# Performance work log

Hardware: AMD Instinct MI355X
Metric: run time of the kernel (lower is better)

## Reference

```python
import jax, jax.numpy as jnp
import numpy as np
from jax import lax

B, C, H, W = 256, 64, 48, 48   # batch, in_channels, spatial_dim, spatial_dim
E = 5                           # num_experts (ConditionalConv2D default)
DIM = 64 + 1                    # n_regulators + 1


def setup_inputs() -> dict:
    key = jax.random.key(0)
    ks = jax.random.split(key, 24)
    def n(k, shape, s=0.05):
        return jax.random.normal(k, shape, jnp.float32) * s
    inp = {
        "spatial_maps": jax.random.normal(ks[0], (B, C, H, W), jnp.float32),
        "cluster_info": jax.random.randint(ks[1], (B,), 0, C),
        # ConditionalConv2D (1x1, num_experts=5)
        "expert_w": n(ks[2], (E, C, C)),          # [experts, out_c, in_c] (1x1 squeezed)
        "cond_b": n(ks[3], (C,)),
        "route_emb": n(ks[4], (C, 4 * C)),        # Embedding(num_clusters=C, pool_emb=4C)
        "route_W": n(ks[5], (E, 8 * C)),          # Linear(2*pool_emb -> E)
        "route_b": n(ks[6], (E,)),
        # weight-normed conv stack (v, g, bias, prelu-a)
        "v1": n(ks[7], (32, C, 3, 3)),  "g1": jnp.ones((32,), jnp.float32),  "cb1": n(ks[8], (32,)),  "a1": jnp.array(0.1, jnp.float32),
        "v2": n(ks[9], (64, 32, 3, 3)), "g2": jnp.ones((64,), jnp.float32),  "cb2": n(ks[10], (64,)), "a2": jnp.array(0.1, jnp.float32),
        "v3": n(ks[11], (128, 64, 3, 3)), "g3": jnp.ones((128,), jnp.float32), "cb3": n(ks[12], (128,)), "a3": jnp.array(0.1, jnp.float32),
        # cluster embedding + alpha + MLP
        "emb2": n(ks[13], (C, 128)),
        "alpha": jnp.array(1.0, jnp.float32),
        "mW1": n(ks[14], (64, 128)), "mb1": n(ks[15], (64,)), "a4": jnp.array(0.1, jnp.float32),
        "mW2": n(ks[16], (32, 64)),  "mb2": n(ks[17], (32,)), "a5": jnp.array(0.1, jnp.float32),
        "mW3": n(ks[18], (DIM, 32)), "mb3": n(ks[19], (DIM,)),
    }
    return inp


def _wn(v, g):
    # weight_norm over all dims except 0 (torch default dim=0)
    nrm = jnp.sqrt((v * v).sum((1, 2, 3)))
    return v * (g / nrm)[:, None, None, None]


def _conv(x, w, b):
    y = lax.conv_general_dilated(x, w, (1, 1), 'SAME',
                                 dimension_numbers=('NCHW', 'OIHW', 'NCHW'))
    return y + b[None, :, None, None]


def _prelu(x, a):
    return jnp.where(x >= 0, x, a * x)


def _mpool(x):
    return lax.reduce_window(x, -jnp.inf, lax.max, (1, 1, 2, 2), (1, 1, 2, 2), 'VALID')


def reference(spatial_maps, cluster_info, expert_w, cond_b, route_emb, route_W, route_b,
              v1, g1, cb1, a1, v2, g2, cb2, a2, v3, g3, cb3, a3,
              emb2, alpha, mW1, mb1, a4, mW2, mb2, a5, mW3, mb3):
    x = spatial_maps
    # routing: adaptive avg pool (2,2), flatten, concat cluster embedding, linear, sigmoid
    pooled = x.reshape(B, C, 2, H // 2, 2, W // 2).mean((3, 5)).reshape(B, 4 * C)
    feat = jnp.concatenate([pooled, route_emb[cluster_info]], axis=1)      # [B, 8C]
    rw = jax.nn.sigmoid(feat @ route_W.T + route_b)                        # [B, E]
    # per-sample expert-mixed 1x1 kernel, applied as batched 1x1 conv
    kern = jnp.einsum('be,eoi->boi', rw, expert_w)                         # [B, C, C]
    cc = jnp.einsum('boi,bihw->bohw', kern, x) + cond_b[None, :, None, None]
    out = jax.nn.sigmoid(cc) * x                                           # attention gate
    # dense conv stack
    h = _mpool(_prelu(_conv(out, _wn(v1, g1), cb1), a1))
    h = _mpool(_prelu(_conv(h, _wn(v2, g2), cb2), a2))
    h = _mpool(_prelu(_conv(h, _wn(v3, g3), cb3), a3))
    h = h.mean((2, 3))                                                      # AdaptiveAvgPool2d(1)+Flatten -> [B,128]
    h = h + emb2[cluster_info] * alpha
    # MLP head
    h = _prelu(h @ mW1.T + mb1, a4)
    h = _prelu(h @ mW2.T + mb2, a5)
    return h @ mW3.T + mb3                                                  # [B, DIM]
```

## Files before the change

### kernel.cpp

```cpp
#include <hip/hip_runtime.h>


typedef _Float16 f16;
typedef f16 f16x8 __attribute__((ext_vector_type(8)));
typedef f16 f16x4 __attribute__((ext_vector_type(4)));
typedef f16 f16x2 __attribute__((ext_vector_type(2)));
typedef __fp16 h16x2 __attribute__((ext_vector_type(2)));
typedef float f32x4 __attribute__((ext_vector_type(4)));

constexpr size_t OFF_POOLED = 0;
constexpr size_t OFF_KERN   = 65536;
constexpr size_t OFF_W1     = 65536 + 1048576;
constexpr size_t OFF_W2     = OFF_W1 + 32*64*12;
constexpr size_t OFF_W3     = OFF_W2 + 64*32*12;
constexpr size_t OFF_H1     = OFF_W3 + 128*64*12;

__device__ __forceinline__ float sigmoidf_(float z) {
    return __builtin_amdgcn_rcpf(1.0f + __expf(-z));
}

__device__ __forceinline__ f16x2 pkrtz(float a, float b) {
    h16x2 r = __builtin_amdgcn_cvt_pkrtz(a, b);
    f16x2 o; o[0] = (f16)r[0]; o[1] = (f16)r[1];
    return o;
}

__device__ __forceinline__ void store_slot8(f16* glds, int row, int sc, int icg, const float* c) {
    f16x2 p0 = pkrtz(c[0], c[1]);
    f16x2 p1 = pkrtz(c[2], c[3]);
    f16x2 p2 = pkrtz(c[4], c[5]);
    f16x2 p3 = pkrtz(c[6], c[7]);
    f16x8 hv = { p0[0], p0[1], p1[0], p1[1], p2[0], p2[1], p3[0], p3[1] };
    *(f16x8*)&glds[(row * 50 + sc) * 64 + ((icg ^ (sc & 7)) << 3)] = hv;
}

__global__ void __launch_bounds__(256)
k_prep(const float* __restrict__ x,
       const float* __restrict__ v1, const float* __restrict__ g1,
       const float* __restrict__ v2, const float* __restrict__ g2,
       const float* __restrict__ v3, const float* __restrict__ g3,
       float* __restrict__ ws)
{
    const int blk = blockIdx.x;
    const int lane = threadIdx.x & 63;
    const int w = threadIdx.x >> 6;
    if (blk < 4096) {
        const int slab = blk * 4 + w;
        const float4* p = (const float4*)(x + (size_t)slab * 2304);
        float a0 = 0.f, a1 = 0.f, a2 = 0.f, a3 = 0.f;
        #pragma unroll
        for (int j = 0; j < 9; j++) {
            int i = lane + 64 * j;
            int row = i / 12, cg = i - 12 * row;
            float4 v = p[i];
            float s = v.x + v.y + v.z + v.w;
            bool hq = (row >= 24), wq = (cg >= 6);
            a0 += (!hq && !wq) ? s : 0.f;
            a1 += (!hq &&  wq) ? s : 0.f;
            a2 += ( hq && !wq) ? s : 0.f;
            a3 += ( hq &&  wq) ? s : 0.f;
        }
        #pragma unroll
        for (int off = 32; off; off >>= 1) {
            a0 += __shfl_down(a0, off);
            a1 += __shfl_down(a1, off);
            a2 += __shfl_down(a2, off);
            a3 += __shfl_down(a3, off);
        }
        if (lane == 0) {
            int b = slab >> 6, c = slab & 63;
            float* d = ws + OFF_POOLED + (size_t)b * 256 + c * 4;
            d[0] = a0 * (1.0f / 576.0f);
            d[1] = a1 * (1.0f / 576.0f);
            d[2] = a2 * (1.0f / 576.0f);
            d[3] = a3 * (1.0f / 576.0f);
        }
    } else {
        int bo = (blk - 4096) * 4 + w;
        const float* v; const float* g; int IC, oc; int which;
        if (bo < 32)       { v = v1; g = g1; oc = bo;      IC = 64; which = 1; }
        else if (bo < 96)  { v = v2; g = g2; oc = bo - 32; IC = 32; which = 2; }
        else               { v = v3; g = g3; oc = bo - 96; IC = 64; which = 3; }
        int n = IC * 9;
        const float* vo = v + (size_t)oc * n;
        float s = 0.0f;
        for (int i = lane; i < n; i += 64) { float xv = vo[i]; s += xv * xv; }
        #pragma unroll
        for (int off = 32; off; off >>= 1) s += __shfl_down(s, off);
        float tot = __shfl(s, 0);
        float sc = g[oc] / sqrtf(tot);
        if (which == 1) {
            f16* o1 = (f16*)(ws + OFF_W1);
            for (int i = lane; i < n; i += 64) {
                int ic = i / 9, kk = i - ic * 9;
                o1[kk * 2048 + oc * 64 + (ic ^ ((oc & 7) << 3))] = (f16)(vo[i] * sc);
            }
        } else if (which == 2) {
            f16* o2 = (f16*)(ws + OFF_W2);
            for (int i = lane; i < n; i += 64) {
                int ic = i / 9, kk = i - ic * 9;
                o2[(kk * 64 + oc) * 32 + ic] = (f16)(vo[i] * sc);
            }
        } else {
            f16* o3 = (f16*)(ws + OFF_W3);
            for (int i = lane; i < n; i += 64) {
                int ic = i / 9, kk = i - ic * 9;
                o3[(kk * 128 + oc) * 64 + ic] = (f16)(vo[i] * sc);
            }
        }
    }
}

__global__ void k_route(const int* __restrict__ cluster,
                        const float* __restrict__ route_emb,
                        const float* __restrict__ route_W,
                        const float* __restrict__ route_b,
                        const float* __restrict__ expert_w,
                        float* __restrict__ ws)
{
    int b = blockIdx.x, t = threadIdx.x;
    __shared__ float feat[512];
    __shared__ float rwv[5];
    __shared__ float red[256];
    int cl = cluster[b];
    feat[t]       = ws[OFF_POOLED + (size_t)b * 256 + t];
    feat[256 + t] = route_emb[(size_t)cl * 256 + t];
    __syncthreads();
    float f0 = feat[t], f1 = feat[256 + t];
    for (int e = 0; e < 5; e++) {
        float pv = f0 * route_W[e * 512 + t] + f1 * route_W[e * 512 + 256 + t];
        red[t] = pv;
        __syncthreads();
        if (t < 128) red[t] += red[t + 128];
        __syncthreads();
        if (t < 64) {
            float s = red[t] + red[t + 64];
            #pragma unroll
            for (int off = 32; off; off >>= 1) s += __shfl_down(s, off);
            if (t == 0) rwv[e] = 1.0f / (1.0f + __expf(-(s + route_b[e])));
        }
        __syncthreads();
    }
    float r0 = rwv[0], r1 = rwv[1], r2 = rwv[2], r3 = rwv[3], r4 = rwv[4];
    f16* khg = (f16*)(ws + OFF_KERN);
    for (int j = t; j < 4096; j += 256) {
        int oc = j >> 6, ic = j & 63;
        float kv = r0 * expert_w[j] + r1 * expert_w[4096 + j] +
                   r2 * expert_w[2 * 4096 + j] + r3 * expert_w[3 * 4096 + j] +
                   r4 * expert_w[4 * 4096 + j];
        khg[(size_t)b * 4096 + oc * 64 + (ic ^ ((oc & 7) << 3))] = (f16)kv;
    }
}

__global__ void __launch_bounds__(512, 4)
k_f1(const float* __restrict__ x, const f16* __restrict__ kernH,
     const float* __restrict__ cond_b, const f16* __restrict__ w1H,
     const float* __restrict__ cb1, const float* __restrict__ a1,
     f16* __restrict__ h1h)
{
    extern __shared__ char smem[];
    f16*  glds  = (f16*)smem;
    f16*  kh    = (f16*)(smem + 64000);
    float* cbl  = (float*)(smem + 72192);
    f16*  hm    = (f16*)smem;

    const int t = threadIdx.x;
    const int tile = blockIdx.x;
    const int b = blockIdx.y;
    const int r0 = tile * 8;
    const int w = t >> 6, l = t & 63;
    const int l15 = l & 15, agrp = l >> 4;

    ((uint4*)kh)[t] = ((const uint4*)(kernH + (size_t)b * 4096))[t];
    if (t < 64) cbl[t] = cond_b[t];
    if (t < 160) {
        int row = t >> 4, rem = t & 15;
        int col = (rem >= 8) ? 49 : 0;
        int slot = rem & 7;
        uint4 z = {};
        *(uint4*)&glds[(row * 50 + col) * 64 + slot * 8] = z;
    }
    for (int e = t; e < 960; e += 512) {
        int row = e / 96;
        int rem = e - row * 96;
        int colg = rem >> 3;
        int icg = rem & 7;
        int r_in = r0 - 1 + row;
        float4 va[8];
        if (r_in >= 0 && r_in < 48) {
            const float4* xp = (const float4*)x + ((size_t)(b * 64 + icg * 8)) * 576 + r_in * 12 + colg;
            #pragma unroll
            for (int i = 0; i < 8; i++) va[i] = xp[i * 576];
        } else {
            #pragma unroll
            for (int i = 0; i < 8; i++) va[i] = (float4){0.f, 0.f, 0.f, 0.f};
        }
        float c0[8], c1[8], c2c[8], c3[8];
        #pragma unroll
        for (int i = 0; i < 8; i++) { c0[i] = va[i].x; c1[i] = va[i].y; c2c[i] = va[i].z; c3[i] = va[i].w; }
        int scb = colg * 4 + 1;
        store_slot8(glds, row, scb + 0, icg, c0);
        store_slot8(glds, row, scb + 1, icg, c1);
        store_slot8(glds, row, scb + 2, icg, c2c);
        store_slot8(glds, row, scb + 3, icg, c3);
    }
    __syncthreads();

    {
        const int nt0 = (w < 6) ? 4 * w : 24 + 3 * (w - 6);
        const int NT  = (w < 6) ? 4 : 3;
        f32x4 acc[4][4] = {};
        int srA[4], scA[4];
        #pragma unroll
        for (int j = 0; j < 4; j++) {
            int ntc = nt0 + ((j < NT) ? j : 0);
            int p = ntc * 16 + l15;
            srA[j] = p / 48; scA[j] = p - 48 * srA[j] + 1;
        }
        #pragma unroll
        for (int ks = 0; ks < 2; ks++) {
            f16x8 kfr[4];
            #pragma unroll
            for (int mt = 0; mt < 4; mt++) {
                int oc = mt * 16 + l15;
                kfr[mt] = *(const f16x8*)&kh[oc * 64 + (((ks * 4 + agrp) ^ (oc & 7)) << 3)];
            }
            #pragma unroll
            for (int j = 0; j < 4; j++) {
                f16x8 bfr = *(const f16x8*)&glds[(srA[j] * 50 + scA[j]) * 64 +
                                                 (((ks * 4 + agrp) ^ (scA[j] & 7)) << 3)];
                #pragma unroll
                for (int mt = 0; mt < 4; mt++)
                    acc[mt][j] = __builtin_amdgcn_mfma_f32_16x16x32_f16(kfr[mt], bfr, acc[mt][j], 0, 0, 0);
            }
        }
        f32x4 cbv[4];
        #pragma unroll
        for (int mt = 0; mt < 4; mt++) cbv[mt] = *(const f32x4*)&cbl[mt * 16 + 4 * agrp];
        #pragma unroll
        for (int j = 0; j < 4; j++) {
            if (j < NT) {
                int base = (srA[j] * 50 + scA[j]) * 64;
                int sw8 = (scA[j] & 7) << 3;
                #pragma unroll
                for (int mt = 0; mt < 4; mt++) {
                    int oc0 = mt * 16 + 4 * agrp;
                    int addr = base + (oc0 ^ sw8);
                    f16x4 xv4 = *(const f16x4*)&glds[addr];
                    float s0 = sigmoidf_(acc[mt][j][0] + cbv[mt][0]);
                    float s1 = sigmoidf_(acc[mt][j][1] + cbv[mt][1]);
                    float s2 = sigmoidf_(acc[mt][j][2] + cbv[mt][2]);
                    float s3 = sigmoidf_(acc[mt][j][3] + cbv[mt][3]);
                    f16x2 slo = pkrtz(s0, s1);
                    f16x2 shi = pkrtz(s2, s3);
                    f16x2 xlo = { xv4[0], xv4[1] };
                    f16x2 xhi = { xv4[2], xv4[3] };
                    f16x2 glo = slo * xlo;
                    f16x2 ghi = shi * xhi;
                    f16x4 g4 = { glo[0], glo[1], ghi[0], ghi[1] };
                    *(f16x4*)&glds[addr] = g4;
                }
            }
        }
    }
    __syncthreads();

    f32x4 c2[3][2] = {};
    {
        const int q = w;
        #pragma unroll
        for (int kt = 0; kt < 18; kt++) {
            const int kk = kt >> 1, hh = kt & 1;
            const int dy = kk / 3, dx = kk - dy * 3;
            f16x8 bfr2[2];
            #pragma unroll
            for (int nt = 0; nt < 2; nt++) {
                int oc = nt * 16 + l15;
                int slot = (hh * 4 + agrp) ^ (oc & 7);
                bfr2[nt] = *(const f16x8*)&w1H[(kk * 32 + oc) * 64 + slot * 8];
            }
            #pragma unroll
            for (int mtl = 0; mtl < 3; mtl++) {
                int sc = mtl * 16 + l15 + dx;
                int slot = (hh * 4 + agrp) ^ (sc & 7);
                f16x8 af = *(const f16x8*)&glds[((q + dy) * 50 + sc) * 64 + slot * 8];
                c2[mtl][0] = __builtin_amdgcn_mfma_f32_16x16x32_f16(af, bfr2[0], c2[mtl][0], 0, 0, 0);
                c2[mtl][1] = __builtin_amdgcn_mfma_f32_16x16x32_f16(af, bfr2[1], c2[mtl][1], 0, 0, 0);
            }
        }
    }
    __syncthreads();

    {
        const int q = w;
        #pragma unroll
        for (int mtl = 0; mtl < 3; mtl++)
            #pragma unroll
            for (int nt = 0; nt < 2; nt++) {
                float h0 = fmaxf(c2[mtl][nt][0], c2[mtl][nt][1]);
                float h1 = fmaxf(c2[mtl][nt][2], c2[mtl][nt][3]);
                f16x2 hp = pkrtz(h0, h1);
                int oc = nt * 16 + l15;
                int pp = mtl * 8 + 2 * agrp;
                *(f16x2*)&hm[(q * 32 + oc) * 26 + pp] = hp;
            }
    }
    __syncthreads();

    {
        const float av = a1[0];
        #pragma unroll
        for (int k = 0; k < 6; k++) {
            int e = t + 512 * k;
            int oc = e & 31, pos2 = e >> 5;
            int pr = pos2 / 24, pc = pos2 - 24 * pr;
            float v0 = (float)hm[((2 * pr) * 32 + oc) * 26 + pc];
            float v1 = (float)hm[((2 * pr + 1) * 32 + oc) * 26 + pc];
            float v = fmaxf(v0, v1) + cb1[oc];
            v = (v >= 0.0f) ? v : av * v;
            h1h[((size_t)b * 576 + tile * 96 + pos2) * 32 + oc] = (f16)v;
        }
    }
}

__global__ void __launch_bounds__(1024, 1)
k_f23(const f16* __restrict__ h1h, const f16* __restrict__ w2h,
      const float* __restrict__ cb2, const float* __restrict__ a2,
      const f16* __restrict__ w3h, const float* __restrict__ cb3, const float* __restrict__ a3,
      const int* __restrict__ cluster, const float* __restrict__ emb2, const float* __restrict__ alpha,
      const float* __restrict__ mW1, const float* __restrict__ mb1, const float* __restrict__ a4,
      const float* __restrict__ mW2, const float* __restrict__ mb2, const float* __restrict__ a5,
      const float* __restrict__ mW3, const float* __restrict__ mb3,
      float* __restrict__ out)
{
    extern __shared__ char smem[];
    f16*  x2    = (f16*)smem;
    f16*  h2l   = (f16*)(smem + 82944);
    float* ps   = (float*)(smem + 111168);
    float* hb   = (float*)(smem + 113216);
    float* t1   = (float*)(smem + 113728);
    float* t2   = (float*)(smem + 113984);
    f16*  dump2 = (f16*)smem;
    f16*  dump3 = (f16*)smem;

    const int b = blockIdx.x, t = threadIdx.x;
    const int w = t >> 6, l = t & 63;
    const int l15 = l & 15, agrp = l >> 4;

    for (int e = t; e < 400; e += 1024) {
        int bp = e >> 2, slot = e & 3;
        int r, c;
        if (bp < 26)      { r = 0;  c = bp; }
        else if (bp < 52) { r = 25; c = bp - 26; }
        else if (bp < 76) { r = bp - 52 + 1; c = 0; }
        else              { r = bp - 76 + 1; c = 25; }
        uint4 z = {};
        *(uint4*)&x2[(r * 26 + c) * 40 + slot * 8] = z;
    }
    for (int e = t; e < 416; e += 1024) {
        int bp = e >> 3, slot = e & 7;
        int r, c;
        if (bp < 14)      { r = 0;  c = bp; }
        else if (bp < 28) { r = 13; c = bp - 14; }
        else if (bp < 40) { r = bp - 28 + 1; c = 0; }
        else              { r = bp - 40 + 1; c = 13; }
        uint4 z = {};
        *(uint4*)&h2l[(r * 14 + c) * 72 + slot * 8] = z;
    }
    {
        const uint4* src = (const uint4*)(h1h + (size_t)b * 18432);
        for (int e = t; e < 2304; e += 1024) {
            int pos = e >> 2, slot = e & 3;
            int r = pos / 24, c = pos - 24 * r;
            *(uint4*)&x2[((r + 1) * 26 + (c + 1)) * 40 + slot * 8] = src[e];
        }
    }
    __syncthreads();

    const int m = w & 3, ng = w >> 2;
    f32x4 acc[9];
    {
        f16x8 afr[9];
        #pragma unroll
        for (int kk = 0; kk < 9; kk++)
            afr[kk] = *(const f16x8*)&w2h[(kk * 64 + m * 16 + l15) * 32 + agrp * 8];
        #pragma unroll
        for (int i = 0; i < 9; i++) acc[i] = (f32x4){0.f, 0.f, 0.f, 0.f};
        constexpr int K2[9] = {0, 40, 80, 26 * 40, 27 * 40, 28 * 40, 52 * 40, 53 * 40, 54 * 40};
        #pragma unroll
        for (int i = 0; i < 9; i++) {
            int p = (ng * 9 + i) * 16 + l15;
            int r = p / 24, c = p - 24 * r;
            int base = (r * 26 + c) * 40 + agrp * 8;
            #pragma unroll
            for (int kk = 0; kk < 9; kk++) {
                f16x8 bfr = *(const f16x8*)&x2[base + K2[kk]];
                acc[i] = __builtin_amdgcn_mfma_f32_16x16x32_f16(afr[kk], bfr, acc[i], 0, 0, 0);
            }
        }
    }
    __syncthreads();

    #pragma unroll
    for (int i = 0; i < 9; i++) {
        int p = (ng * 9 + i) * 16 + l15;
        f16x2 d0 = pkrtz(acc[i][0], acc[i][1]);
        f16x2 d1 = pkrtz(acc[i][2], acc[i][3]);
        f16x4 hv = { d0[0], d0[1], d1[0], d1[1] };
        *(f16x4*)&dump2[p * 72 + m * 16 + 4 * agrp] = hv;
    }
    __syncthreads();

    {
        const float a2v = a2[0];
        for (int e = t; e < 9216; e += 1024) {
            int oc = e & 63, pos2 = e >> 6;
            int pr = pos2 / 12, pc = pos2 - 12 * pr;
            int p0 = (2 * pr) * 24 + 2 * pc;
            float mm = fmaxf(fmaxf((float)dump2[p0 * 72 + oc], (float)dump2[(p0 + 1) * 72 + oc]),
                             fmaxf((float)dump2[(p0 + 24) * 72 + oc], (float)dump2[(p0 + 25) * 72 + oc]));
            float v = mm + cb2[oc];
            v = (v >= 0.0f) ? v : a2v * v;
            h2l[((pr + 1) * 14 + (pc + 1)) * 72 + oc] = (f16)v;
        }
    }
    __syncthreads();

    const int m8 = w & 7, ng3 = w >> 3;
    const int nt0c3 = ng3 * 5;
    const int cnt3  = ng3 ? 4 : 5;
    f32x4 acc3[5];
    {
        int pb[5];
        #pragma unroll
        for (int i = 0; i < 5; i++) {
            int p = (nt0c3 + i) * 16 + l15;
            int r = p / 12, c = p - 12 * r;
            pb[i] = ((r + 1) * 14 + (c + 1)) * 72 + agrp * 8;
            acc3[i] = (f32x4){0.f, 0.f, 0.f, 0.f};
        }
        constexpr int K3[9] = {-15 * 72, -14 * 72, -13 * 72, -72, 0, 72, 13 * 72, 14 * 72, 15 * 72};
        #pragma unroll
        for (int kk = 0; kk < 9; kk++) {
            #pragma unroll
            for (int ks = 0; ks < 2; ks++) {
                f16x8 afr = *(const f16x8*)&w3h[(size_t)(kk * 128 + m8 * 16 + l15) * 64 + ks * 32 + agrp * 8];
                #pragma unroll
                for (int i = 0; i < 5; i++) {
                    if (i < cnt3) {
                        f16x8 bfr = *(const f16x8*)&h2l[pb[i] + ks * 32 + K3[kk]];
                        acc3[i] = __builtin_amdgcn_mfma_f32_16x16x32_f16(afr, bfr, acc3[i], 0, 0, 0);
                    }
                }
            }
        }
    }
    #pragma unroll
    for (int i = 0; i < 5; i++) {
        if (i < cnt3) {
            int p = (nt0c3 + i) * 16 + l15;
            f16x2 d0 = pkrtz(acc3[i][0], acc3[i][1]);
            f16x2 d1 = pkrtz(acc3[i][2], acc3[i][3]);
            f16x4 hv = { d0[0], d0[1], d1[0], d1[1] };
            *(f16x4*)&dump3[p * 136 + m8 * 16 + 4 * agrp] = hv;
        }
    }
    __syncthreads();

    if (t < 512) {
        int oc = t >> 2, q = t & 3;
        int qr = q >> 1, qc = q & 1;
        const float a3v = a3[0];
        float cbv = cb3[oc];
        float s = 0.f;
        #pragma unroll
        for (int i = 0; i < 3; i++)
            #pragma unroll
            for (int j = 0; j < 3; j++) {
                int pr = 3 * qr + i, pc = 3 * qc + j;
                int p0 = (2 * pr) * 12 + 2 * pc;
                float mm = fmaxf(fmaxf((float)dump3[p0 * 136 + oc], (float)dump3[(p0 + 1) * 136 + oc]),
                                 fmaxf((float)dump3[(p0 + 12) * 136 + oc], (float)dump3[(p0 + 13) * 136 + oc]));
                float v = mm + cbv;
                v = (v >= 0.0f) ? v : a3v * v;
                s += v;
            }
        ps[t] = s;
    }
    __syncthreads();
    if (t < 128) {
        int cl = cluster[b];
        hb[t] = (ps[4 * t] + ps[4 * t + 1] + ps[4 * t + 2] + ps[4 * t + 3]) * (1.0f / 36.0f)
              + emb2[(size_t)cl * 128 + t] * alpha[0];
    }
    __syncthreads();
    if (t < 64) {
        const float4* wr = (const float4*)(mW1 + t * 128);
        float s = mb1[t];
        #pragma unroll 8
        for (int j = 0; j < 32; j++) {
            float4 wv4 = wr[j];
            s += wv4.x * hb[4 * j] + wv4.y * hb[4 * j + 1] + wv4.z * hb[4 * j + 2] + wv4.w * hb[4 * j + 3];
        }
        float a4v = a4[0];
        t1[t] = (s >= 0.0f) ? s : a4v * s;
    }
    __syncthreads();
    if (t < 32) {
        const float4* wr = (const float4*)(mW2 + t * 64);
        float s = mb2[t];
        #pragma unroll
        for (int j = 0; j < 16; j++) {
            float4 wv4 = wr[j];
            s += wv4.x * t1[4 * j] + wv4.y * t1[4 * j + 1] + wv4.z * t1[4 * j + 2] + wv4.w * t1[4 * j + 3];
        }
        float a5v = a5[0];
        t2[t] = (s >= 0.0f) ? s : a5v * s;
    }
    __syncthreads();
    if (t < 65) {
        const float4* wr = (const float4*)(mW3 + t * 32);
        float s = mb3[t];
        #pragma unroll
        for (int j = 0; j < 8; j++) {
            float4 wv4 = wr[j];
            s += wv4.x * t2[4 * j] + wv4.y * t2[4 * j + 1] + wv4.z * t2[4 * j + 2] + wv4.w * t2[4 * j + 3];
        }
        out[(size_t)b * 65 + t] = s;
    }
}

extern "C" void kernel_launch(void* const* d_in, const int* in_sizes, int n_in,
                              void* d_out, int out_size, void* d_ws, size_t ws_size,
                              hipStream_t stream)
{
    const float* x         = (const float*)d_in[0];
    const int*   cluster   = (const int*)  d_in[1];
    const float* expert_w  = (const float*)d_in[2];
    const float* cond_b    = (const float*)d_in[3];
    const float* route_emb = (const float*)d_in[4];
    const float* route_W   = (const float*)d_in[5];
    const float* route_b   = (const float*)d_in[6];
    const float* v1  = (const float*)d_in[7];
    const float* g1  = (const float*)d_in[8];
    const float* cb1 = (const float*)d_in[9];
    const float* a1  = (const float*)d_in[10];
    const float* v2  = (const float*)d_in[11];
    const float* g2  = (const float*)d_in[12];
    const float* cb2 = (const float*)d_in[13];
    const float* a2  = (const float*)d_in[14];
    const float* v3  = (const float*)d_in[15];
    const float* g3  = (const float*)d_in[16];
    const float* cb3 = (const float*)d_in[17];
    const float* a3  = (const float*)d_in[18];
    const float* emb2  = (const float*)d_in[19];
    const float* alpha = (const float*)d_in[20];
    const float* mW1 = (const float*)d_in[21];
    const float* mb1 = (const float*)d_in[22];
    const float* a4  = (const float*)d_in[23];
    const float* mW2 = (const float*)d_in[24];
    const float* mb2 = (const float*)d_in[25];
    const float* a5  = (const float*)d_in[26];
    const float* mW3 = (const float*)d_in[27];
    const float* mb3 = (const float*)d_in[28];
    float* ws  = (float*)d_ws;
    float* out = (float*)d_out;

    hipFuncSetAttribute((const void*)k_f1,  hipFuncAttributeMaxDynamicSharedMemorySize, 72448);
    hipFuncSetAttribute((const void*)k_f23, hipFuncAttributeMaxDynamicSharedMemorySize, 114112);

    k_prep<<<4152, 256, 0, stream>>>(x, v1, g1, v2, g2, v3, g3, ws);
    k_route<<<256, 256, 0, stream>>>(cluster, route_emb, route_W, route_b, expert_w, ws);
    k_f1<<<dim3(6, 256), 512, 72448, stream>>>(x, (const f16*)(ws + OFF_KERN), cond_b,
                                               (const f16*)(ws + OFF_W1), cb1, a1,
                                               (f16*)(ws + OFF_H1));
    k_f23<<<256, 1024, 114112, stream>>>((const f16*)(ws + OFF_H1), (const f16*)(ws + OFF_W2),
                                         cb2, a2, (const f16*)(ws + OFF_W3), cb3, a3,
                                         cluster, emb2, alpha,
                                         mW1, mb1, a4, mW2, mb2, a5, mW3, mb3, out);
}
```

Before: 118.7 us.

## Pre-convert input to swizzled fp16 NHWC in prep pass, load via LDS DMA

The prep kernel now reads x once, writes an fp16 channel-last copy with the LDS swizzle already applied, and stores per-row partial sums for the routing pool. The first conv kernel then fills shared memory with direct global-to-LDS loads of that fp16 copy instead of converting fp32 x itself, and routing sums the per-row partials. This aims to halve the bytes the conv kernel reads and drop conversion work from it. In exchange it adds an extra fp16 write and read of the whole input in workspace, plus a fallback to the old path when the workspace is too small.

```diff
diff --git a/kernel.cpp b/kernel.cpp
--- a/kernel.cpp
+++ b/kernel.cpp
@@ -14,6 +14,9 @@
 constexpr size_t OFF_W2     = OFF_W1 + 32*64*12;
 constexpr size_t OFF_W3     = OFF_W2 + 64*32*12;
 constexpr size_t OFF_H1     = OFF_W3 + 128*64*12;
+constexpr size_t OFF_XH     = OFF_H1 + (size_t)256*576*32/2;
+constexpr size_t OFF_PP     = OFF_XH + (size_t)256*48*48*64/2;
+constexpr size_t WS_NEED    = OFF_PP + (size_t)256*48*128;
 
 __device__ __forceinline__ float sigmoidf_(float z) {
     return __builtin_amdgcn_rcpf(1.0f + __expf(-z));
@@ -25,21 +28,315 @@
     return o;
 }
 
-__device__ __forceinline__ void store_slot8(f16* glds, int row, int sc, int icg, const float* c) {
+__device__ __forceinline__ f16x8 pk8(const float* c) {
     f16x2 p0 = pkrtz(c[0], c[1]);
     f16x2 p1 = pkrtz(c[2], c[3]);
     f16x2 p2 = pkrtz(c[4], c[5]);
     f16x2 p3 = pkrtz(c[6], c[7]);
     f16x8 hv = { p0[0], p0[1], p1[0], p1[1], p2[0], p2[1], p3[0], p3[1] };
-    *(f16x8*)&glds[(row * 50 + sc) * 64 + ((icg ^ (sc & 7)) << 3)] = hv;
+    return hv;
+}
+
+__device__ __forceinline__ void store_slot8(f16* glds, int row, int sc, int icg, const float* c) {
+    *(f16x8*)&glds[(row * 50 + sc) * 64 + ((icg ^ (sc & 7)) << 3)] = pk8(c);
+}
+
+__device__ __forceinline__ void wnorm_one(int bo, int lane,
+    const float* v1, const float* g1, const float* v2, const float* g2,
+    const float* v3, const float* g3, float* ws)
+{
+    const float* v; const float* g; int IC, oc; int which;
+    if (bo < 32)       { v = v1; g = g1; oc = bo;      IC = 64; which = 1; }
+    else if (bo < 96)  { v = v2; g = g2; oc = bo - 32; IC = 32; which = 2; }
+    else               { v = v3; g = g3; oc = bo - 96; IC = 64; which = 3; }
+    int n = IC * 9;
+    const float* vo = v + (size_t)oc * n;
+    float s = 0.0f;
+    for (int i = lane; i < n; i += 64) { float xv = vo[i]; s += xv * xv; }
+    #pragma unroll
+    for (int off = 32; off; off >>= 1) s += __shfl_down(s, off);
+    float tot = __shfl(s, 0);
+    float sc = g[oc] / sqrtf(tot);
+    if (which == 1) {
+        f16* o1 = (f16*)(ws + OFF_W1);
+        for (int i = lane; i < n; i += 64) {
+            int ic = i / 9, kk = i - ic * 9;
+            o1[kk * 2048 + oc * 64 + (ic ^ ((oc & 7) << 3))] = (f16)(vo[i] * sc);
+        }
+    } else if (which == 2) {
+        f16* o2 = (f16*)(ws + OFF_W2);
+        for (int i = lane; i < n; i += 64) {
+            int ic = i / 9, kk = i - ic * 9;
+            o2[(kk * 64 + oc) * 32 + ic] = (f16)(vo[i] * sc);
+        }
+    } else {
+        f16* o3 = (f16*)(ws + OFF_W3);
+        for (int i = lane; i < n; i += 64) {
+            int ic = i / 9, kk = i - ic * 9;
+            o3[(kk * 128 + oc) * 64 + ic] = (f16)(vo[i] * sc);
+        }
+    }
+}
+
+__global__ void __launch_bounds__(128)
+k_prep_x(const float* __restrict__ x,
+         const float* __restrict__ v1, const float* __restrict__ g1,
+         const float* __restrict__ v2, const float* __restrict__ g2,
+         const float* __restrict__ v3, const float* __restrict__ g3,
+         float* __restrict__ ws)
+{
+    const int blk = blockIdx.x;
+    const int t = threadIdx.x;
+    if (blk < 12288) {
+        const int b = blk / 48, row = blk - 48 * b;
+        __shared__ float part[12][64];
+        f16* xh = (f16*)(ws + OFF_XH);
+        if (t < 96) {
+            const int icg = t & 7, colg = t >> 3;
+            const float4* xp = (const float4*)x + ((size_t)(b * 64 + icg * 8)) * 576 + row * 12 + colg;
+            float4 va[8];
+            #pragma unroll
+            for (int i = 0; i < 8; i++) va[i] = xp[i * 576];
+            float c0[8], c1[8], c2c[8], c3[8];
+            #pragma unroll
+            for (int i = 0; i < 8; i++) { c0[i] = va[i].x; c1[i] = va[i].y; c2c[i] = va[i].z; c3[i] = va[i].w; }
+            size_t xb = ((size_t)b * 48 + row) * 48;
+            int g0 = colg * 4;
+            *(f16x8*)&xh[(xb + g0 + 0) * 64 + ((icg ^ ((g0 + 1) & 7)) << 3)] = pk8(c0);
+            *(f16x8*)&xh[(xb + g0 + 1) * 64 + ((icg ^ ((g0 + 2) & 7)) << 3)] = pk8(c1);
+            *(f16x8*)&xh[(xb + g0 + 2) * 64 + ((icg ^ ((g0 + 3) & 7)) << 3)] = pk8(c2c);
+            *(f16x8*)&xh[(xb + g0 + 3) * 64 + ((icg ^ ((g0 + 4) & 7)) << 3)] = pk8(c3);
+            #pragma unroll
+            for (int i = 0; i < 8; i++)
+                part[colg][icg * 8 + i] = va[i].x + va[i].y + va[i].z + va[i].w;
+        }
+        __syncthreads();
+        {
+            int ch = t & 63, wq = t >> 6;
+            float s = 0.f;
+            #pragma unroll
+            for (int j = 0; j < 6; j++) s += part[wq * 6 + j][ch];
+            ws[OFF_PP + ((size_t)b * 48 + row) * 128 + wq * 64 + ch] = s * (1.0f / 576.0f);
+        }
+    } else {
+        if (t < 64) wnorm_one(blk - 12288, t, v1, g1, v2, g2, v3, g3, ws);
+    }
+}
+
+__global__ void k_route_n(const int* __restrict__ cluster,
+                          const float* __restrict__ route_emb,
+                          const float* __restrict__ route_W,
+                          const float* __restrict__ route_b,
+                          const float* __restrict__ expert_w,
+                          float* __restrict__ ws)
+{
+    int b = blockIdx.x, t = threadIdx.x;
+    __shared__ float feat[512];
+    __shared__ float rwv[5];
+    __shared__ float red[256];
+    int cl = cluster[b];
+    {
+        int c = t >> 2, quad = t & 3;
+        int hb_ = quad >> 1, wb_ = quad & 1;
+        const float* pp = ws + OFF_PP + ((size_t)b * 48 + hb_ * 24) * 128 + wb_ * 64 + c;
+        float s = 0.f;
+        #pragma unroll 8
+        for (int r = 0; r < 24; r++) s += pp[r * 128];
+        feat[t] = s;
+    }
+    feat[256 + t] = route_emb[(size_t)cl * 256 + t];
+    __syncthreads();
+    float f0 = feat[t], f1 = feat[256 + t];
+    for (int e = 0; e < 5; e++) {
+        float pv = f0 * route_W[e * 512 + t] + f1 * route_W[e * 512 + 256 + t];
+        red[t] = pv;
+        __syncthreads();
+        if (t < 128) red[t] += red[t + 128];
+        __syncthreads();
+        if (t < 64) {
+            float s = red[t] + red[t + 64];
+            #pragma unroll
+            for (int off = 32; off; off >>= 1) s += __shfl_down(s, off);
+            if (t == 0) rwv[e] = 1.0f / (1.0f + __expf(-(s + route_b[e])));
+        }
+        __syncthreads();
+    }
+    float r0 = rwv[0], r1 = rwv[1], r2 = rwv[2], r3 = rwv[3], r4 = rwv[4];
+    f16* khg = (f16*)(ws + OFF_KERN);
+    for (int j = t; j < 4096; j += 256) {
+        int oc = j >> 6, ic = j & 63;
+        float kv = r0 * expert_w[j] + r1 * expert_w[4096 + j] +
+                   r2 * expert_w[2 * 4096 + j] + r3 * expert_w[3 * 4096 + j] +
+                   r4 * expert_w[4 * 4096 + j];
+        khg[(size_t)b * 4096 + oc * 64 + (ic ^ ((oc & 7) << 3))] = (f16)kv;
+    }
+}
+
+__global__ void __launch_bounds__(512, 4)
+k_f1_n(const f16* __restrict__ xh, const f16* __restrict__ kernH,
+       const float* __restrict__ cond_b, const f16* __restrict__ w1H,
+       const float* __restrict__ cb1, const float* __restrict__ a1,
+       f16* __restrict__ h1h)
+{
+    extern __shared__ char smem[];
+    f16*  glds  = (f16*)smem;
+    f16*  kh    = (f16*)(smem + 64000);
+    float* cbl  = (float*)(smem + 72192);
+    f16*  hm    = (f16*)smem;
+
+    const int t = threadIdx.x;
+    const int tile = blockIdx.x;
+    const int b = blockIdx.y;
+    const int r0 = tile * 8;
+    const int w = t >> 6, l = t & 63;
+    const int l15 = l & 15, agrp = l >> 4;
+
+    ((uint4*)kh)[t] = ((const uint4*)(kernH + (size_t)b * 4096))[t];
+    if (t < 64) cbl[t] = cond_b[t];
+    if (t < 160) {
+        int row = t >> 4, rem = t & 15;
+        int col = (rem >= 8) ? 49 : 0;
+        int slot = rem & 7;
+        uint4 z = {};
+        *(uint4*)&glds[(row * 50 + col) * 64 + slot * 8] = z;
+    }
+    for (int e2 = w; e2 < 60; e2 += 8) {
+        int row = e2 / 6, seg = e2 - 6 * row;
+        int r_in = r0 - 1 + row;
+        f16* dst = glds + (row * 50 + 1) * 64 + seg * 512;
+        if (r_in >= 0 && r_in < 48) {
+            const f16* src = xh + ((size_t)b * 48 + r_in) * 3072 + seg * 512 + l * 8;
+            __builtin_amdgcn_global_load_lds((const uint32_t*)src, (uint32_t*)dst, 16, 0, 0);
+        } else {
+            uint4 z = {};
+            *(uint4*)&dst[l * 8] = z;
+        }
+    }
+    __syncthreads();
+
+    {
+        const int nt0 = (w < 6) ? 4 * w : 24 + 3 * (w - 6);
+        const int NT  = (w < 6) ? 4 : 3;
+        f32x4 acc[4][4] = {};
+        int srA[4], scA[4];
+        #pragma unroll
+        for (int j = 0; j < 4; j++) {
+            int ntc = nt0 + ((j < NT) ? j : 0);
+            int p = ntc * 16 + l15;
+            srA[j] = p / 48; scA[j] = p - 48 * srA[j] + 1;
+        }
+        #pragma unroll
+        for (int ks = 0; ks < 2; ks++) {
+            f16x8 kfr[4];
+            #pragma unroll
+            for (int mt = 0; mt < 4; mt++) {
+                int oc = mt * 16 + l15;
+                kfr[mt] = *(const f16x8*)&kh[oc * 64 + (((ks * 4 + agrp) ^ (oc & 7)) << 3)];
+            }
+            #pragma unroll
+            for (int j = 0; j < 4; j++) {
+                f16x8 bfr = *(const f16x8*)&glds[(srA[j] * 50 + scA[j]) * 64 +
+                                                 (((ks * 4 + agrp) ^ (scA[j] & 7)) << 3)];
+                #pragma unroll
+                for (int mt = 0; mt < 4; mt++)
+                    acc[mt][j] = __builtin_amdgcn_mfma_f32_16x16x32_f16(kfr[mt], bfr, acc[mt][j], 0, 0, 0);
+            }
+        }
+        f32x4 cbv[4];
+        #pragma unroll
+        for (int mt = 0; mt < 4; mt++) cbv[mt] = *(const f32x4*)&cbl[mt * 16 + 4 * agrp];
+        #pragma unroll
+        for (int j = 0; j < 4; j++) {
+            if (j < NT) {
+                int base = (srA[j] * 50 + scA[j]) * 64;
+                int sw8 = (scA[j] & 7) << 3;
+                #pragma unroll
+                for (int mt = 0; mt < 4; mt++) {
+                    int oc0 = mt * 16 + 4 * agrp;
+                    int addr = base + (oc0 ^ sw8);
+                    f16x4 xv4 = *(const f16x4*)&glds[addr];
+                    float s0 = sigmoidf_(acc[mt][j][0] + cbv[mt][0]);
+                    float s1 = sigmoidf_(acc[mt][j][1] + cbv[mt][1]);
+                    float s2 = sigmoidf_(acc[mt][j][2] + cbv[mt][2]);
+                    float s3 = sigmoidf_(acc[mt][j][3] + cbv[mt][3]);
+                    f16x2 slo = pkrtz(s0, s1);
+                    f16x2 shi = pkrtz(s2, s3);
+                    f16x2 xlo = { xv4[0], xv4[1] };
+                    f16x2 xhi = { xv4[2], xv4[3] };
+                    f16x2 glo = slo * xlo;
+                    f16x2 ghi = shi * xhi;
+                    f16x4 g4 = { glo[0], glo[1], ghi[0], ghi[1] };
+                    *(f16x4*)&glds[addr] = g4;
+                }
+            }
+        }
+    }
+    __syncthreads();
+
+    f32x4 c2[3][2] = {};
+    {
+        const int q = w;
+        #pragma unroll
+        for (int kt = 0; kt < 18; kt++) {
+            const int kk = kt >> 1, hh = kt & 1;
+            const int dy = kk / 3, dx = kk - dy * 3;
+            f16x8 bfr2[2];
+            #pragma unroll
+            for (int nt = 0; nt < 2; nt++) {
+                int oc = nt * 16 + l15;
+                int slot = (hh * 4 + agrp) ^ (oc & 7);
+                bfr2[nt] = *(const f16x8*)&w1H[(kk * 32 + oc) * 64 + slot * 8];
+            }
+            #pragma unroll
+            for (int mtl = 0; mtl < 3; mtl++) {
+                int sc = mtl * 16 + l15 + dx;
+                int slot = (hh * 4 + agrp) ^ (sc & 7);
+                f16x8 af = *(const f16x8*)&glds[((q + dy) * 50 + sc) * 64 + slot * 8];
+                c2[mtl][0] = __builtin_amdgcn_mfma_f32_16x16x32_f16(af, bfr2[0], c2[mtl][0], 0, 0, 0);
+                c2[mtl][1] = __builtin_amdgcn_mfma_f32_16x16x32_f16(af, bfr2[1], c2[mtl][1], 0, 0, 0);
+            }
+        }
+    }
+    __syncthreads();
+
+    {
+        const int q = w;
+        #pragma unroll
+        for (int mtl = 0; mtl < 3; mtl++)
+            #pragma unroll
+            for (int nt = 0; nt < 2; nt++) {
+                float h0 = fmaxf(c2[mtl][nt][0], c2[mtl][nt][1]);
+                float h1 = fmaxf(c2[mtl][nt][2], c2[mtl][nt][3]);
+                f16x2 hp = pkrtz(h0, h1);
+                int oc = nt * 16 + l15;
+                int pp = mtl * 8 + 2 * agrp;
+                *(f16x2*)&hm[(q * 32 + oc) * 26 + pp] = hp;
+            }
+    }
+    __syncthreads();
+
+    {
+        const float av = a1[0];
+        #pragma unroll
+        for (int k = 0; k < 6; k++) {
+            int e = t + 512 * k;
+            int oc = e & 31, pos2 = e >> 5;
+            int pr = pos2 / 24, pc = pos2 - 24 * pr;
+            float v0 = (float)hm[((2 * pr) * 32 + oc) * 26 + pc];
+            float v1 = (float)hm[((2 * pr + 1) * 32 + oc) * 26 + pc];
+            float v = fmaxf(v0, v1) + cb1[oc];
+            v = (v >= 0.0f) ? v : av * v;
+            h1h[((size_t)b * 576 + tile * 96 + pos2) * 32 + oc] = (f16)v;
+        }
+    }
 }
 
 __global__ void __launch_bounds__(256)
-k_prep(const float* __restrict__ x,
-       const float* __restrict__ v1, const float* __restrict__ g1,
-       const float* __restrict__ v2, const float* __restrict__ g2,
-       const float* __restrict__ v3, const float* __restrict__ g3,
-       float* __restrict__ ws)
+k_prep_o(const float* __restrict__ x,
+         const float* __restrict__ v1, const float* __restrict__ g1,
+         const float* __restrict__ v2, const float* __restrict__ g2,
+         const float* __restrict__ v3, const float* __restrict__ g3,
+         float* __restrict__ ws)
 {
     const int blk = blockIdx.x;
     const int lane = threadIdx.x & 63;
@@ -76,47 +373,16 @@
             d[3] = a3 * (1.0f / 576.0f);
         }
     } else {
-        int bo = (blk - 4096) * 4 + w;
-        const float* v; const float* g; int IC, oc; int which;
-        if (bo < 32)       { v = v1; g = g1; oc = bo;      IC = 64; which = 1; }
-        else if (bo < 96)  { v = v2; g = g2; oc = bo - 32; IC = 32; which = 2; }
-        else               { v = v3; g = g3; oc = bo - 96; IC = 64; which = 3; }
-        int n = IC * 9;
-        const float* vo = v + (size_t)oc * n;
-        float s = 0.0f;
-        for (int i = lane; i < n; i += 64) { float xv = vo[i]; s += xv * xv; }
-        #pragma unroll
-        for (int off = 32; off; off >>= 1) s += __shfl_down(s, off);
-        float tot = __shfl(s, 0);
-        float sc = g[oc] / sqrtf(tot);
-        if (which == 1) {
-            f16* o1 = (f16*)(ws + OFF_W1);
-            for (int i = lane; i < n; i += 64) {
-                int ic = i / 9, kk = i - ic * 9;
-                o1[kk * 2048 + oc * 64 + (ic ^ ((oc & 7) << 3))] = (f16)(vo[i] * sc);
-            }
-        } else if (which == 2) {
-            f16* o2 = (f16*)(ws + OFF_W2);
-            for (int i = lane; i < n; i += 64) {
-                int ic = i / 9, kk = i - ic * 9;
-                o2[(kk * 64 + oc) * 32 + ic] = (f16)(vo[i] * sc);
-            }
-        } else {
-            f16* o3 = (f16*)(ws + OFF_W3);
-            for (int i = lane; i < n; i += 64) {
-                int ic = i / 9, kk = i - ic * 9;
-                o3[(kk * 128 + oc) * 64 + ic] = (f16)(vo[i] * sc);
-            }
-        }
-    }
-}
-
-__global__ void k_route(const int* __restrict__ cluster,
-                        const float* __restrict__ route_emb,
-                        const float* __restrict__ route_W,
-                        const float* __restrict__ route_b,
-                        const float* __restrict__ expert_w,
-                        float* __restrict__ ws)
+        wnorm_one((blk - 4096) * 4 + w, lane, v1, g1, v2, g2, v3, g3, ws);
+    }
+}
+
+__global__ void k_route_o(const int* __restrict__ cluster,
+                          const float* __restrict__ route_emb,
+                          const float* __restrict__ route_W,
+                          const float* __restrict__ route_b,
+                          const float* __restrict__ expert_w,
+                          float* __restrict__ ws)
 {
     int b = blockIdx.x, t = threadIdx.x;
     __shared__ float feat[512];
@@ -153,10 +419,10 @@
 }
 
 __global__ void __launch_bounds__(512, 4)
-k_f1(const float* __restrict__ x, const f16* __restrict__ kernH,
-     const float* __restrict__ cond_b, const f16* __restrict__ w1H,
-     const float* __restrict__ cb1, const float* __restrict__ a1,
-     f16* __restrict__ h1h)
+k_f1_o(const float* __restrict__ x, const f16* __restrict__ kernH,
+       const float* __restrict__ cond_b, const f16* __restrict__ w1H,
+       const float* __restrict__ cb1, const float* __restrict__ a1,
+       f16* __restrict__ h1h)
 {
     extern __shared__ char smem[];
     f16*  glds  = (f16*)smem;
@@ -566,14 +832,26 @@
     float* ws  = (float*)d_ws;
     float* out = (float*)d_out;
 
-    hipFuncSetAttribute((const void*)k_f1,  hipFuncAttributeMaxDynamicSharedMemorySize, 72448);
-    hipFuncSetAttribute((const void*)k_f23, hipFuncAttributeMaxDynamicSharedMemorySize, 114112);
-
-    k_prep<<<4152, 256, 0, stream>>>(x, v1, g1, v2, g2, v3, g3, ws);
-    k_route<<<256, 256, 0, stream>>>(cluster, route_emb, route_W, route_b, expert_w, ws);
-    k_f1<<<dim3(6, 256), 512, 72448, stream>>>(x, (const f16*)(ws + OFF_KERN), cond_b,
-                                               (const f16*)(ws + OFF_W1), cb1, a1,
-                                               (f16*)(ws + OFF_H1));
+    hipFuncSetAttribute((const void*)k_f1_n, hipFuncAttributeMaxDynamicSharedMemorySize, 72448);
+    hipFuncSetAttribute((const void*)k_f1_o, hipFuncAttributeMaxDynamicSharedMemorySize, 72448);
+    hipFuncSetAttribute((const void*)k_f23,  hipFuncAttributeMaxDynamicSharedMemorySize, 114112);
+
+    const bool big_ws = (ws_size >= WS_NEED * sizeof(float));
+
+    if (big_ws) {
+        k_prep_x<<<12512, 128, 0, stream>>>(x, v1, g1, v2, g2, v3, g3, ws);
+        k_route_n<<<256, 256, 0, stream>>>(cluster, route_emb, route_W, route_b, expert_w, ws);
+        k_f1_n<<<dim3(6, 256), 512, 72448, stream>>>((const f16*)(ws + OFF_XH),
+                                                     (const f16*)(ws + OFF_KERN), cond_b,
+                                                     (const f16*)(ws + OFF_W1), cb1, a1,
+                                                     (f16*)(ws + OFF_H1));
+    } else {
+        k_prep_o<<<4152, 256, 0, stream>>>(x, v1, g1, v2, g2, v3, g3, ws);
+        k_route_o<<<256, 256, 0, stream>>>(cluster, route_emb, route_W, route_b, expert_w, ws);
+        k_f1_o<<<dim3(6, 256), 512, 72448, stream>>>(x, (const f16*)(ws + OFF_KERN), cond_b,
+                                                     (const f16*)(ws + OFF_W1), cb1, a1,
+                                                     (f16*)(ws + OFF_H1));
+    }
     k_f23<<<256, 1024, 114112, stream>>>((const f16*)(ws + OFF_H1), (const f16*)(ws + OFF_W2),
                                          cb2, a2, (const f16*)(ws + OFF_W3), cb3, a3,
                                          cluster, emb2, alpha,
```

After: 129.2 us. +8.8%, slower.
